# Kernel optimization log

Hardware: AMD Instinct MI355X
Metric: run time of the kernel (lower is better)

## Reference

```python
import jax, jax.numpy as jnp
import numpy as np

B, T, N, A, D, S, E, H = 32, 64, 16, 20, 128, 32, 64, 256  # batch, time, n_agents, n_actions, state_dim, sample_size, embed_dim, hypernet_embed


def _lin(k, fi, fo):
    return jax.random.normal(k, (fi, fo), jnp.float32) / np.sqrt(fi)


def setup_inputs() -> dict:
    key = jax.random.key(0)
    ks = jax.random.split(key, 16)
    batch = B * T
    states = jax.random.normal(ks[0], (B, T, D), jnp.float32)
    a_idx = jax.random.randint(ks[1], (B, T, N), 0, A)
    actions = jax.nn.one_hot(a_idx, A, dtype=jnp.float32)
    agent_qs = jax.random.normal(ks[2], (B, T, N), jnp.float32)
    max_filter = jnp.zeros((B, T, N), jnp.float32)
    # random agent permutations (torch.multinomial without replacement)
    grand_coalitions = jnp.argsort(jax.random.uniform(ks[3], (batch * S, N)), axis=1).astype(jnp.int32)
    return {
        "states": states, "actions": actions, "agent_qs": agent_qs,
        "max_filter": max_filter, "grand_coalitions": grand_coalitions,
        # hyper_w_1: Linear(D,H) -> ReLU -> Linear(H, E*2A)
        "W1a": _lin(ks[4], D, H), "b1a": jnp.zeros((H,), jnp.float32),
        "W1b": _lin(ks[5], H, E * 2 * A), "b1b": jnp.zeros((E * 2 * A,), jnp.float32),
        # hyper_b_1: Linear(D,E)
        "Wb": _lin(ks[6], D, E), "bb": jnp.zeros((E,), jnp.float32),
        # hyper_w_final: Linear(D,H) -> ReLU -> Linear(H,E)
        "Wfa": _lin(ks[7], D, H), "bfa": jnp.zeros((H,), jnp.float32),
        "Wfb": _lin(ks[8], H, E), "bfb": jnp.zeros((E,), jnp.float32),
        # V: Linear(D,E) -> ReLU -> Linear(E,1)
        "Wv1": _lin(ks[9], D, E), "bv1": jnp.zeros((E,), jnp.float32),
        "Wv2": _lin(ks[10], E, 1), "bv2": jnp.zeros((1,), jnp.float32),
    }


def reference(states, actions, agent_qs, max_filter, grand_coalitions,
              W1a, b1a, W1b, b1b, Wb, bb, Wfa, bfa, Wfb, bfb, Wv1, bv1, Wv2, bv2):
    b, t = states.shape[0], states.shape[1]
    batch = b * t
    n, a = actions.shape[2], actions.shape[3]
    s = grand_coalitions.shape[0] // batch
    e = Wb.shape[1]

    st = states.reshape(batch, -1)                      # [batch, D]
    act = actions.reshape(batch, n, a)                  # [batch, N, A]
    gc = grand_coalitions.reshape(batch, s, n)          # [batch, S, N]

    # individual_map one-hot + tril matmul => subcoalition; mask = sub - ind = (j < gc)
    j = jnp.arange(n)
    sub = (j[None, None, None, :] <= gc[..., None]).astype(st.dtype)   # [batch,S,N,N]
    ind = (j[None, None, None, :] == gc[..., None]).astype(st.dtype)
    mask = sub - ind                                                    # [batch,S,i,j]

    # gathered (permuted) actions: perm_act[b,s,j,:] = act[b, gc[b,s,j], :]
    perm_act = act[jnp.arange(batch)[:, None, None], gc]                # [batch,S,N,A]

    # mean over coalition axis j of masked actions, times coalition size, mean over samples
    numer = jnp.einsum('bsij,bsja->bsia', mask, perm_act)               # sum_j masked actions
    cnt = mask.sum(-1)                                                  # [batch,S,N]
    coal = ((numer / n) * cnt[..., None]).mean(axis=1)                  # [batch,N,A]

    # per (batch, agent) hypernetwork mixing
    inputs = jnp.concatenate([coal, act], axis=-1).reshape(batch * n, 2 * a)  # [bn, 2A]
    st_rep = jnp.broadcast_to(st[:, None, :], (batch, n, st.shape[-1])).reshape(batch * n, -1)

    def mlp2(x, Wa_, ba_, Wb_, bb_):
        return jax.nn.relu(x @ Wa_ + ba_) @ Wb_ + bb_

    w1 = jnp.abs(mlp2(st_rep, W1a, b1a, W1b, b1b)).reshape(-1, 2 * a, e)      # [bn,2A,E]
    b1 = (st_rep @ Wb + bb)                                                   # [bn,E]
    hidden = jax.nn.elu(jnp.einsum('bk,bke->be', inputs, w1) + b1)            # [bn,E]
    w_final = jnp.abs(mlp2(st_rep, Wfa, bfa, Wfb, bfb))                       # [bn,E]
    v = jax.nn.relu(st_rep @ Wv1 + bv1) @ Wv2 + bv2                           # [bn,1]
    y = jnp.sum(hidden * w_final, axis=-1, keepdims=True) + v                 # [bn,1]
    w_est = jnp.abs(y).reshape(b, t, n)

    q_tot = jnp.sum(w_est * agent_qs, axis=2, keepdims=True)                  # [B,T,1]
    return q_tot, w_est
```

## Files before the change

### kernel.cpp

```cpp
#include <hip/hip_runtime.h>
#include <math.h>


#define BATCH 2048

typedef __attribute__((ext_vector_type(8))) short bf16x8;
typedef __attribute__((ext_vector_type(4))) float f32x4;

__device__ inline unsigned short f2bf(float f) {
    unsigned int u = __float_as_uint(f);
    unsigned int r = (u + 0x7FFFu + ((u >> 16) & 1u)) >> 16;
    return (unsigned short)r;
}
__device__ inline float bf2f(unsigned short s) {
    return __uint_as_float(((unsigned int)s) << 16);
}

__global__ __launch_bounds__(256) void k1(
    const float* __restrict__ X,
    const float* __restrict__ W1a, const float* __restrict__ b1a,
    const float* __restrict__ Wfa, const float* __restrict__ bfa,
    const float* __restrict__ Wb,  const float* __restrict__ bb,
    const float* __restrict__ Wv1, const float* __restrict__ bv1,
    const float* __restrict__ W1b,
    unsigned short* __restrict__ h1_bf, float* __restrict__ hf,
    float* __restrict__ b1buf, float* __restrict__ vrelu,
    unsigned short* __restrict__ Bp)
{
    __shared__ float As[16][64];
    __shared__ float Bs[16][64];
    const int t = threadIdx.x, bid = blockIdx.x;

    if (bid >= 320) {
        int idx = (bid - 320) * 256 + t;
        int n_local = idx & 127;
        int g = idx >> 7;
        int kg = g & 3, kcn = g >> 2;
        int kc = kcn & 7, nb = kcn >> 3;
        int kbase = kc * 32 + kg * 8;
        int col = nb * 128 + n_local;
        unsigned short o[8];
        #pragma unroll
        for (int j = 0; j < 8; ++j)
            o[j] = f2bf(W1b[(kbase + j) * 2560 + col]);
        *(uint4*)&Bp[idx * 8] = *(uint4*)o;
        return;
    }

    const int nb = bid % 10, mb = bid / 10;
    const int m0 = mb * 64, n0 = nb * 64;
    const int tx = t & 15, ty = t >> 4;
    const int lm = t >> 2, lk = (t & 3) << 2;
    const int lkk = t >> 4, lnb = (t & 15) << 2;

    const float* Wsrc; const float* bsrc; int ldb, c0;
    if (nb < 4)       { Wsrc = W1a; bsrc = b1a; ldb = 256; c0 = n0; }
    else if (nb < 8)  { Wsrc = Wfa; bsrc = bfa; ldb = 256; c0 = n0 - 256; }
    else if (nb == 8) { Wsrc = Wb;  bsrc = bb;  ldb = 64;  c0 = 0; }
    else              { Wsrc = Wv1; bsrc = bv1; ldb = 64;  c0 = 0; }

    float c[4][4] = {{0}};
    for (int k0 = 0; k0 < 128; k0 += 16) {
        float4 av = *(const float4*)&X[(m0 + lm) * 128 + k0 + lk];
        As[lk][lm] = av.x; As[lk+1][lm] = av.y; As[lk+2][lm] = av.z; As[lk+3][lm] = av.w;
        *(float4*)&Bs[lkk][lnb] = *(const float4*)&Wsrc[(k0 + lkk) * ldb + c0 + lnb];
        __syncthreads();
        #pragma unroll
        for (int kk = 0; kk < 16; ++kk) {
            float4 a4 = *(const float4*)&As[kk][ty * 4];
            float4 b4 = *(const float4*)&Bs[kk][tx * 4];
            float aa[4] = {a4.x, a4.y, a4.z, a4.w};
            float bb4[4] = {b4.x, b4.y, b4.z, b4.w};
            #pragma unroll
            for (int i = 0; i < 4; ++i)
                #pragma unroll
                for (int j = 0; j < 4; ++j)
                    c[i][j] = fmaf(aa[i], bb4[j], c[i][j]);
        }
        __syncthreads();
    }
    const int ncol = c0 + tx * 4;
    float4 bias = *(const float4*)&bsrc[ncol];
    #pragma unroll
    for (int i = 0; i < 4; ++i) {
        int m = m0 + ty * 4 + i;
        float v0 = c[i][0] + bias.x, v1 = c[i][1] + bias.y;
        float v2 = c[i][2] + bias.z, v3 = c[i][3] + bias.w;
        if (nb < 4) {
            ushort4 o;
            o.x = f2bf(fmaxf(v0, 0.f)); o.y = f2bf(fmaxf(v1, 0.f));
            o.z = f2bf(fmaxf(v2, 0.f)); o.w = f2bf(fmaxf(v3, 0.f));
            *(ushort4*)&h1_bf[m * 256 + ncol] = o;
        } else if (nb < 8) {
            float4 o = { fmaxf(v0,0.f), fmaxf(v1,0.f), fmaxf(v2,0.f), fmaxf(v3,0.f) };
            *(float4*)&hf[m * 256 + ncol] = o;
        } else if (nb == 8) {
            float4 o = { v0, v1, v2, v3 };
            *(float4*)&b1buf[m * 64 + ncol] = o;
        } else {
            float4 o = { fmaxf(v0,0.f), fmaxf(v1,0.f), fmaxf(v2,0.f), fmaxf(v3,0.f) };
            *(float4*)&vrelu[m * 64 + ncol] = o;
        }
    }
}

#define AS_STRIDE 40
__global__ __launch_bounds__(256) void k2(
    const unsigned short* __restrict__ A, const unsigned short* __restrict__ Bp,
    const float* __restrict__ bias, unsigned short* __restrict__ C,
    const float* __restrict__ hf, const float* __restrict__ Wfb,
    const float* __restrict__ bfb, float* __restrict__ wf)
{
    __shared__ __align__(16) char smem[18432];
    const int t = threadIdx.x, bid = blockIdx.x;

    if (bid < 320) {
        unsigned short* As = (unsigned short*)smem;
        unsigned short* Bs = (unsigned short*)(smem + 10240);
        const int lane = t & 63, wave = t >> 6;
        const int ln15 = lane & 15, q4 = lane >> 4;
        const int nb = bid % 20, m0 = (bid / 20) * 128, n0 = nb * 128;
        const int wm = (wave & 1) * 64, wn = (wave >> 1) * 64;

        f32x4 acc[4][4];
        #pragma unroll
        for (int i = 0; i < 4; ++i)
            #pragma unroll
            for (int j = 0; j < 4; ++j)
                acc[i][j] = (f32x4){0.f, 0.f, 0.f, 0.f};

        for (int kc = 0; kc < 8; ++kc) {
            #pragma unroll
            for (int c = 0; c < 2; ++c) {
                int ch = t + c * 256;
                int row = ch >> 2, part = ch & 3;
                *(uint4*)&As[row * AS_STRIDE + part * 8] =
                    *(const uint4*)&A[(m0 + row) * 256 + kc * 32 + part * 8];
            }
            {
                const uint4* src = (const uint4*)&Bp[(nb * 8 + kc) * 4096];
                ((uint4*)Bs)[t] = src[t];
                ((uint4*)Bs)[t + 256] = src[t + 256];
            }
            __syncthreads();
            bf16x8 af[4], bfr[4];
            #pragma unroll
            for (int mi = 0; mi < 4; ++mi)
                af[mi] = *(const bf16x8*)&As[(wm + mi * 16 + ln15) * AS_STRIDE + q4 * 8];
            #pragma unroll
            for (int ni = 0; ni < 4; ++ni)
                bfr[ni] = *(const bf16x8*)&Bs[(q4 * 128 + wn + ni * 16 + ln15) * 8];
            #pragma unroll
            for (int mi = 0; mi < 4; ++mi)
                #pragma unroll
                for (int ni = 0; ni < 4; ++ni)
                    acc[mi][ni] = __builtin_amdgcn_mfma_f32_16x16x32_bf16(af[mi], bfr[ni], acc[mi][ni], 0, 0, 0);
            __syncthreads();
        }
        #pragma unroll
        for (int ni = 0; ni < 4; ++ni) {
            int col = n0 + wn + ni * 16 + ln15;
            float bv = bias[col];
            #pragma unroll
            for (int mi = 0; mi < 4; ++mi) {
                #pragma unroll
                for (int j = 0; j < 4; ++j) {
                    int row = m0 + wm + mi * 16 + q4 * 4 + j;
                    C[row * 2560 + col] = f2bf(fabsf(acc[mi][ni][j] + bv));
                }
            }
        }
    } else {
        float* hfs  = (float*)smem;
        float* wfbs = (float*)(smem + 2048);
        const int e = t & 63, mg = t >> 6;
        const int b0 = (bid - 320) * 8;
        float acc0 = 0.f, acc1 = 0.f;

        for (int kc = 0; kc < 4; ++kc) {
            for (int i = t; i < 1024; i += 256)
                ((float4*)wfbs)[i] = ((const float4*)(Wfb + kc * 64 * 64))[i];
            if (t < 128) {
                int r = t >> 4, p = t & 15;
                ((float4*)hfs)[t] = *(const float4*)&hf[(b0 + r) * 256 + kc * 64 + p * 4];
            }
            __syncthreads();
            #pragma unroll 8
            for (int k = 0; k < 64; ++k) {
                float wv = wfbs[k * 64 + e];
                acc0 = fmaf(hfs[mg * 64 + k], wv, acc0);
                acc1 = fmaf(hfs[(mg + 4) * 64 + k], wv, acc1);
            }
            __syncthreads();
        }
        float bf = bfb[e];
        wf[(b0 + mg) * 64 + e]     = fabsf(acc0 + bf);
        wf[(b0 + mg + 4) * 64 + e] = fabsf(acc1 + bf);
    }
}

__global__ __launch_bounds__(1024) void k3(
    const float* __restrict__ actions, const int* __restrict__ gc,
    const unsigned short* __restrict__ w1, const float* __restrict__ b1buf,
    const float* __restrict__ wf, const float* __restrict__ vrelu,
    const float* __restrict__ Wv2, const float* __restrict__ bv2,
    const float* __restrict__ agent_qs, float* __restrict__ out)
{
    __shared__ float ins[16][20];
    __shared__ unsigned short w1s[1280];
    __shared__ int aidx[16];
    __shared__ int q[32][16];
    __shared__ unsigned int msk[32][20];
    __shared__ float wq[16];
    const int t = threadIdx.x, b = blockIdx.x;

    if (t < 160) {
        ((uint4*)w1s)[t] = ((const uint4*)(w1 + b * 2560))[t];
    } else if (t < 480) {
        int u = t - 160;
        float av = actions[b * 320 + u];
        if (av > 0.5f) aidx[u / 20] = u % 20;
    } else if (t < 608) {
        ((uint4*)q)[t - 480] = ((const uint4*)(gc + b * 512))[t - 480];
    } else if (t < 768) {
        ((uint4*)msk)[t - 608] = make_uint4(0u, 0u, 0u, 0u);
    }
    __syncthreads();

    if (t >= 512) {
        int u = t - 512, s = u >> 4, j = u & 15;
        atomicOr(&msk[s][aidx[q[s][j]]], 1u << j);
    }
    __syncthreads();

    if (t < 320) {
        int i = t / 20, a = t % 20;
        float acc = 0.f;
        #pragma unroll 8
        for (int s = 0; s < 32; ++s) {
            int g = q[s][i];
            acc += (float)(g * __popc(msk[s][a] & ((1u << g) - 1u)));
        }
        ins[i][a] = acc * (1.0f / 512.0f);
    }
    __syncthreads();

    const int i = t >> 6, e = t & 63;
    float acc = b1buf[b * 64 + e];
    #pragma unroll
    for (int k = 0; k < 20; ++k)
        acc = fmaf(ins[i][k], bf2f(w1s[k * 64 + e]), acc);
    acc += bf2f(w1[b * 2560 + (20 + aidx[i]) * 64 + e]);
    float hidden = acc > 0.f ? acc : expm1f(acc);
    float p = hidden * wf[b * 64 + e] + vrelu[b * 64 + e] * Wv2[e];
    #pragma unroll
    for (int off = 32; off > 0; off >>= 1)
        p += __shfl_down(p, off, 64);
    if (e == 0) {
        float west = fabsf(p + bv2[0]);
        out[2048 + b * 16 + i] = west;
        wq[i] = west * agent_qs[b * 16 + i];
    }
    __syncthreads();
    if (t == 0) {
        float s = 0.f;
        #pragma unroll
        for (int ii = 0; ii < 16; ++ii) s += wq[ii];
        out[b] = s;
    }
}

extern "C" void kernel_launch(void* const* d_in, const int* in_sizes, int n_in,
                              void* d_out, int out_size, void* d_ws, size_t ws_size,
                              hipStream_t stream) {
    const float* states   = (const float*)d_in[0];
    const float* actions  = (const float*)d_in[1];
    const float* agent_qs = (const float*)d_in[2];
    const int*   gc       = (const int*)d_in[4];
    const float* W1a = (const float*)d_in[5];
    const float* b1a = (const float*)d_in[6];
    const float* W1b = (const float*)d_in[7];
    const float* b1b = (const float*)d_in[8];
    const float* Wb  = (const float*)d_in[9];
    const float* bb  = (const float*)d_in[10];
    const float* Wfa = (const float*)d_in[11];
    const float* bfa = (const float*)d_in[12];
    const float* Wfb = (const float*)d_in[13];
    const float* bfb = (const float*)d_in[14];
    const float* Wv1 = (const float*)d_in[15];
    const float* bv1 = (const float*)d_in[16];
    const float* Wv2 = (const float*)d_in[17];
    const float* bv2 = (const float*)d_in[18];

    float* ws     = (float*)d_ws;
    float* hf     = ws;
    float* b1buf  = hf + 524288;
    float* vrelu  = b1buf + 131072;
    float* wfbuf  = vrelu + 131072;
    unsigned short* h1_bf = (unsigned short*)(wfbuf + 131072);
    unsigned short* Bp    = h1_bf + 524288;
    unsigned short* w1    = Bp + 655360;
    float* out = (float*)d_out;

    k1<<<640, 256, 0, stream>>>(states, W1a, b1a, Wfa, bfa, Wb, bb, Wv1, bv1,
                                W1b, h1_bf, hf, b1buf, vrelu, Bp);
    k2<<<576, 256, 0, stream>>>(h1_bf, Bp, b1b, w1, hf, Wfb, bfb, wfbuf);
    k3<<<BATCH, 1024, 0, stream>>>(actions, gc, w1, b1buf, wfbuf, vrelu,
                                   Wv2, bv2, agent_qs, out);
}
```

Baseline: 137.0 us.

## Restructure k3 to four batches per block and load full K tile in k1

k3 now processes four batch rows per 256-thread block, with one wavefront per batch looping over the 16 agents. The whole 2560-element w1 slice is staged in shared memory, so the action-indexed w1 row no longer needs a separate global load, and the cross-wave reduction through shared memory is replaced by a per-wave accumulation. The aim is to cut 1024-thread block overhead and idle threads. k1 now loads the entire 128-deep A and B tiles into shared memory in one pass, with a swizzled A layout, removing the per-16-k synchronisation. The larger shared memory footprint in both kernels (64 KB in k1) may reduce occupancy.

```diff
diff --git a/kernel.cpp b/kernel.cpp
--- a/kernel.cpp
+++ b/kernel.cpp
@@ -15,6 +15,7 @@
 __device__ inline float bf2f(unsigned short s) {
     return __uint_as_float(((unsigned int)s) << 16);
 }
+__device__ inline int aswz(int m, int k) { return (k + 4 * m) & 127; }
 
 __global__ __launch_bounds__(256) void k1(
     const float* __restrict__ X,
@@ -27,8 +28,8 @@
     float* __restrict__ b1buf, float* __restrict__ vrelu,
     unsigned short* __restrict__ Bp)
 {
-    __shared__ float As[16][64];
-    __shared__ float Bs[16][64];
+    __shared__ float As[64][128];
+    __shared__ float Bs[128][64];
     const int t = threadIdx.x, bid = blockIdx.x;
 
     if (bid >= 320) {
@@ -50,8 +51,6 @@
     const int nb = bid % 10, mb = bid / 10;
     const int m0 = mb * 64, n0 = nb * 64;
     const int tx = t & 15, ty = t >> 4;
-    const int lm = t >> 2, lk = (t & 3) << 2;
-    const int lkk = t >> 4, lnb = (t & 15) << 2;
 
     const float* Wsrc; const float* bsrc; int ldb, c0;
     if (nb < 4)       { Wsrc = W1a; bsrc = b1a; ldb = 256; c0 = n0; }
@@ -59,33 +58,51 @@
     else if (nb == 8) { Wsrc = Wb;  bsrc = bb;  ldb = 64;  c0 = 0; }
     else              { Wsrc = Wv1; bsrc = bv1; ldb = 64;  c0 = 0; }
 
-    float c[4][4] = {{0}};
-    for (int k0 = 0; k0 < 128; k0 += 16) {
-        float4 av = *(const float4*)&X[(m0 + lm) * 128 + k0 + lk];
-        As[lk][lm] = av.x; As[lk+1][lm] = av.y; As[lk+2][lm] = av.z; As[lk+3][lm] = av.w;
-        *(float4*)&Bs[lkk][lnb] = *(const float4*)&Wsrc[(k0 + lkk) * ldb + c0 + lnb];
-        __syncthreads();
-        #pragma unroll
-        for (int kk = 0; kk < 16; ++kk) {
-            float4 a4 = *(const float4*)&As[kk][ty * 4];
-            float4 b4 = *(const float4*)&Bs[kk][tx * 4];
-            float aa[4] = {a4.x, a4.y, a4.z, a4.w};
-            float bb4[4] = {b4.x, b4.y, b4.z, b4.w};
+    #pragma unroll
+    for (int c = 0; c < 8; ++c) {
+        int idx = t + c * 256;
+        int row = idx >> 5, f4c = idx & 31;
+        float4 v = *(const float4*)&X[(m0 + row) * 128 + f4c * 4];
+        *(float4*)&As[row][aswz(row, f4c * 4)] = v;
+    }
+    #pragma unroll
+    for (int c = 0; c < 8; ++c) {
+        int idx = t + c * 256;
+        int row = idx >> 4, f4c = idx & 15;
+        *(float4*)&Bs[row][f4c * 4] = *(const float4*)&Wsrc[row * ldb + c0 + f4c * 4];
+    }
+    __syncthreads();
+
+    float acc[4][4] = {{0}};
+    for (int kb = 0; kb < 128; kb += 4) {
+        float av[4][4], bv4[4][4];
+        #pragma unroll
+        for (int i = 0; i < 4; ++i) {
+            int m = ty * 4 + i;
+            float4 v = *(const float4*)&As[m][aswz(m, kb)];
+            av[i][0] = v.x; av[i][1] = v.y; av[i][2] = v.z; av[i][3] = v.w;
+        }
+        #pragma unroll
+        for (int kk = 0; kk < 4; ++kk) {
+            float4 v = *(const float4*)&Bs[kb + kk][tx * 4];
+            bv4[kk][0] = v.x; bv4[kk][1] = v.y; bv4[kk][2] = v.z; bv4[kk][3] = v.w;
+        }
+        #pragma unroll
+        for (int kk = 0; kk < 4; ++kk)
             #pragma unroll
             for (int i = 0; i < 4; ++i)
                 #pragma unroll
                 for (int j = 0; j < 4; ++j)
-                    c[i][j] = fmaf(aa[i], bb4[j], c[i][j]);
-        }
-        __syncthreads();
-    }
+                    acc[i][j] = fmaf(av[i][kk], bv4[kk][j], acc[i][j]);
+    }
+
     const int ncol = c0 + tx * 4;
     float4 bias = *(const float4*)&bsrc[ncol];
     #pragma unroll
     for (int i = 0; i < 4; ++i) {
         int m = m0 + ty * 4 + i;
-        float v0 = c[i][0] + bias.x, v1 = c[i][1] + bias.y;
-        float v2 = c[i][2] + bias.z, v3 = c[i][3] + bias.w;
+        float v0 = acc[i][0] + bias.x, v1 = acc[i][1] + bias.y;
+        float v2 = acc[i][2] + bias.z, v3 = acc[i][3] + bias.w;
         if (nb < 4) {
             ushort4 o;
             o.x = f2bf(fmaxf(v0, 0.f)); o.y = f2bf(fmaxf(v1, 0.f));
@@ -199,75 +216,97 @@
     }
 }
 
-__global__ __launch_bounds__(1024) void k3(
+__global__ __launch_bounds__(256) void k3(
     const float* __restrict__ actions, const int* __restrict__ gc,
     const unsigned short* __restrict__ w1, const float* __restrict__ b1buf,
     const float* __restrict__ wf, const float* __restrict__ vrelu,
     const float* __restrict__ Wv2, const float* __restrict__ bv2,
     const float* __restrict__ agent_qs, float* __restrict__ out)
 {
-    __shared__ float ins[16][20];
-    __shared__ unsigned short w1s[1280];
-    __shared__ int aidx[16];
-    __shared__ int q[32][16];
-    __shared__ unsigned int msk[32][20];
-    __shared__ float wq[16];
-    const int t = threadIdx.x, b = blockIdx.x;
-
-    if (t < 160) {
-        ((uint4*)w1s)[t] = ((const uint4*)(w1 + b * 2560))[t];
-    } else if (t < 480) {
-        int u = t - 160;
-        float av = actions[b * 320 + u];
-        if (av > 0.5f) aidx[u / 20] = u % 20;
-    } else if (t < 608) {
-        ((uint4*)q)[t - 480] = ((const uint4*)(gc + b * 512))[t - 480];
-    } else if (t < 768) {
-        ((uint4*)msk)[t - 608] = make_uint4(0u, 0u, 0u, 0u);
+    __shared__ unsigned short w1s[4][2560];
+    __shared__ float ins[4][16][20];
+    __shared__ int aidx[4][16];
+    __shared__ int q[4][32][16];
+    __shared__ unsigned int msk[4][32][20];
+    const int t = threadIdx.x;
+    const int b0 = blockIdx.x * 4;
+
+    #pragma unroll
+    for (int r = 0; r < 5; ++r) {
+        int idx = t + r * 256;
+        int bb = idx / 320, off = idx % 320;
+        ((uint4*)w1s[bb])[off] = ((const uint4*)(w1 + (b0 + bb) * 2560))[off];
+    }
+    #pragma unroll
+    for (int r = 0; r < 2; ++r) {
+        int idx = t + r * 256;
+        int bb = idx >> 7, off = idx & 127;
+        ((uint4*)q[bb])[off] = ((const uint4*)(gc + (b0 + bb) * 512))[off];
+    }
+    #pragma unroll
+    for (int r = 0; r < 3; ++r) {
+        int idx = t + r * 256;
+        if (idx < 640) ((uint4*)msk)[idx] = make_uint4(0u, 0u, 0u, 0u);
+    }
+    #pragma unroll
+    for (int r = 0; r < 5; ++r) {
+        int idx = t + r * 256;
+        int bb = idx / 320, u = idx % 320;
+        float av = actions[(b0 + bb) * 320 + u];
+        if (av > 0.5f) aidx[bb][u / 20] = u % 20;
     }
     __syncthreads();
 
-    if (t >= 512) {
-        int u = t - 512, s = u >> 4, j = u & 15;
-        atomicOr(&msk[s][aidx[q[s][j]]], 1u << j);
+    #pragma unroll
+    for (int r = 0; r < 8; ++r) {
+        int u = t + r * 256;
+        int bb = u >> 9, s = (u >> 4) & 31, j = u & 15;
+        atomicOr(&msk[bb][s][aidx[bb][q[bb][s][j]]], 1u << j);
     }
     __syncthreads();
 
-    if (t < 320) {
-        int i = t / 20, a = t % 20;
+    #pragma unroll
+    for (int r = 0; r < 5; ++r) {
+        int u = t + r * 256;
+        int bb = u / 320, v = u % 320;
+        int i = v / 20, a = v % 20;
         float acc = 0.f;
         #pragma unroll 8
         for (int s = 0; s < 32; ++s) {
-            int g = q[s][i];
-            acc += (float)(g * __popc(msk[s][a] & ((1u << g) - 1u)));
-        }
-        ins[i][a] = acc * (1.0f / 512.0f);
+            int g = q[bb][s][i];
+            acc += (float)(g * __popc(msk[bb][s][a] & ((1u << g) - 1u)));
+        }
+        ins[bb][i][a] = acc * (1.0f / 512.0f);
     }
     __syncthreads();
 
-    const int i = t >> 6, e = t & 63;
-    float acc = b1buf[b * 64 + e];
-    #pragma unroll
-    for (int k = 0; k < 20; ++k)
-        acc = fmaf(ins[i][k], bf2f(w1s[k * 64 + e]), acc);
-    acc += bf2f(w1[b * 2560 + (20 + aidx[i]) * 64 + e]);
-    float hidden = acc > 0.f ? acc : expm1f(acc);
-    float p = hidden * wf[b * 64 + e] + vrelu[b * 64 + e] * Wv2[e];
-    #pragma unroll
-    for (int off = 32; off > 0; off >>= 1)
-        p += __shfl_down(p, off, 64);
-    if (e == 0) {
-        float west = fabsf(p + bv2[0]);
-        out[2048 + b * 16 + i] = west;
-        wq[i] = west * agent_qs[b * 16 + i];
-    }
-    __syncthreads();
-    if (t == 0) {
-        float s = 0.f;
-        #pragma unroll
-        for (int ii = 0; ii < 16; ++ii) s += wq[ii];
-        out[b] = s;
-    }
+    const int wv = t >> 6, e = t & 63;
+    const int b = b0 + wv;
+    const float b1v = b1buf[b * 64 + e];
+    const float wfv = wf[b * 64 + e];
+    const float vv  = vrelu[b * 64 + e] * Wv2[e];
+    const float aq  = (e < 16) ? agent_qs[b * 16 + e] : 0.f;
+    const float bv2v = bv2[0];
+    float qtot = 0.f;
+    for (int i = 0; i < 16; ++i) {
+        float acc = b1v;
+        #pragma unroll
+        for (int k = 0; k < 20; ++k)
+            acc = fmaf(ins[wv][i][k], bf2f(w1s[wv][k * 64 + e]), acc);
+        acc += bf2f(w1s[wv][(20 + aidx[wv][i]) * 64 + e]);
+        float hidden = acc > 0.f ? acc : expm1f(acc);
+        float p = hidden * wfv + vv;
+        #pragma unroll
+        for (int off = 32; off > 0; off >>= 1)
+            p += __shfl_down(p, off, 64);
+        float aqi = __shfl(aq, i, 64);
+        if (e == 0) {
+            float west = fabsf(p + bv2v);
+            out[2048 + b * 16 + i] = west;
+            qtot = fmaf(west, aqi, qtot);
+        }
+    }
+    if (e == 0) out[b] = qtot;
 }
 
 extern "C" void kernel_launch(void* const* d_in, const int* in_sizes, int n_in,
@@ -305,6 +344,6 @@
     k1<<<640, 256, 0, stream>>>(states, W1a, b1a, Wfa, bfa, Wb, bb, Wv1, bv1,
                                 W1b, h1_bf, hf, b1buf, vrelu, Bp);
     k2<<<576, 256, 0, stream>>>(h1_bf, Bp, b1b, w1, hf, Wfb, bfb, wfbuf);
-    k3<<<BATCH, 1024, 0, stream>>>(actions, gc, w1, b1buf, wfbuf, vrelu,
-                                   Wv2, bv2, agent_qs, out);
-}
+    k3<<<512, 256, 0, stream>>>(actions, gc, w1, b1buf, wfbuf, vrelu,
+                                Wv2, bv2, agent_qs, out);
+}
```

New measurement: 137.1 us. No clear change (+0.1%).
